# Optimization experiments

Measured on AMD Instinct MI355X. Metric: run time of the kernel, lower is better.

## Reference

```python
import jax, jax.numpy as jnp
import numpy as np

C, H, W = 32, 128, 128

def grid_sample_plane(plane, gx, gy):
    """PyTorch F.grid_sample(mode='bilinear', align_corners=True, padding_mode='zeros').
    plane: (C,H,W); gx,gy: (B,N) in [-1,1] (x indexes W, y indexes H).
    Returns (B,C,N)."""
    x = (gx + 1.0) * 0.5 * (W - 1)
    y = (gy + 1.0) * 0.5 * (H - 1)
    x0 = jnp.floor(x); y0 = jnp.floor(y)
    wx = x - x0; wy = y - y0
    x0i = x0.astype(jnp.int32); y0i = y0.astype(jnp.int32)
    def corner(xi, yi, w):
        valid = (xi >= 0) & (xi < W) & (yi >= 0) & (yi < H)
        xc = jnp.clip(xi, 0, W - 1); yc = jnp.clip(yi, 0, H - 1)
        v = plane[:, yc, xc]            # (C,B,N)
        return v * (w * valid)[None]
    out = (corner(x0i, y0i, (1 - wx) * (1 - wy))
           + corner(x0i + 1, y0i, wx * (1 - wy))
           + corner(x0i, y0i + 1, (1 - wx) * wy)
           + corner(x0i + 1, y0i + 1, wx * wy))   # (C,B,N)
    return jnp.transpose(out, (1, 0, 2))           # (B,C,N)


def setup_inputs() -> dict:
    key = jax.random.key(0)
    ks = jax.random.split(key, 8)
    B, N = 4, 262144
    grid_coords = jax.random.uniform(ks[0], (B, N, 3), jnp.float32, -1.0, 1.0)
    triplanes = jax.random.normal(ks[1], (3 * C, H, W), jnp.float32)
    w0 = jax.random.normal(ks[2], (128, 32), jnp.float32) * (1.0 / np.sqrt(32))
    b0 = jax.random.normal(ks[3], (128,), jnp.float32) * 0.01
    w1 = jax.random.normal(ks[4], (128, 128), jnp.float32) * (1.0 / np.sqrt(128))
    b1 = jax.random.normal(ks[5], (128,), jnp.float32) * 0.01
    w2 = jax.random.normal(ks[6], (4, 128), jnp.float32) * (1.0 / np.sqrt(128))
    b2 = jax.random.normal(ks[7], (4,), jnp.float32) * 0.01
    return {"grid_coords": grid_coords, "triplanes": triplanes,
            "w0": w0, "b0": b0, "w1": w1, "b1": b1, "w2": w2, "b2": b2}


def reference(grid_coords, triplanes, w0, b0, w1, b1, w2, b2):
    B, N, _ = grid_coords.shape
    feat_xy, feat_yz, feat_xz = jnp.split(triplanes, 3, axis=0)
    x = grid_coords[..., 0]; y = grid_coords[..., 1]; z = grid_coords[..., 2]
    # fused tri-plane gather + sum, (B,C,N)
    sampled = (grid_sample_plane(feat_xy, x, y)
               + grid_sample_plane(feat_xz, x, z)
               + grid_sample_plane(feat_yz, y, z))
    # NOTE: the original code does .reshape(batch, -1, channel) on a (B,C,1,N)
    # contiguous tensor (NOT a transpose) -- replicate that exact layout reinterpretation.
    feats = sampled.reshape(B, N, C)
    net = jax.nn.relu(feats @ w0.T + b0)
    net = jax.nn.relu(net @ w1.T + b1)
    net = jax.nn.relu(net @ w2.T + b2)            # (B,N,4)
    # raw = cat(rgb=net[...,1:4], alpha=net[...,0:1]) along channel
    raw = jnp.concatenate([net[..., 1:4], net[..., 0:1]], axis=-1)
    return raw
```

## Files before the change

### kernel.cpp

```cpp
#include <hip/hip_runtime.h>
#include <hip/hip_bf16.h>


#define C_ 32
#define HW_ (128 * 128)
#define HQS 40

typedef short s8v __attribute__((ext_vector_type(8)));
typedef float f4v __attribute__((ext_vector_type(4)));
typedef unsigned int u4v __attribute__((ext_vector_type(4)));
typedef unsigned int u2v __attribute__((ext_vector_type(2)));

__device__ __attribute__((aligned(64))) unsigned short g_planes[3 * HW_ * C_];
__device__ __attribute__((aligned(16))) unsigned short g_w0[128 * 32];
__device__ __attribute__((aligned(16))) unsigned short g_w1[128 * 128];
__device__ __attribute__((aligned(16))) unsigned short g_w2[16 * 128];
__device__ __attribute__((aligned(16))) float g_b0[128];
__device__ __attribute__((aligned(16))) float g_b1[128];
__device__ __attribute__((aligned(16))) float g_b2p[16];

template <typename TO, typename FROM>
static __device__ __forceinline__ TO bitc(FROM f) {
    union { FROM a; TO b; } u; u.a = f; return u.b;
}

template <typename V>
static __device__ __forceinline__ auto mfma_k32(V a, V b, f4v c, int)
    -> decltype(__builtin_amdgcn_mfma_f32_16x16x32_bf16(a, b, c, 0, 0, 0)) {
    return __builtin_amdgcn_mfma_f32_16x16x32_bf16(a, b, c, 0, 0, 0);
}
template <typename V>
static __device__ __forceinline__ f4v mfma_k32(V a, V b, f4v c, long) {
    typedef __bf16 b8v __attribute__((ext_vector_type(8)));
    return __builtin_amdgcn_mfma_f32_16x16x32_bf16(bitc<b8v>(a), bitc<b8v>(b), c, 0, 0, 0);
}
static __device__ __forceinline__ f4v MFMA(s8v a, s8v b, f4v c) {
    return mfma_k32(a, b, c, 0);
}

__device__ __forceinline__ unsigned short f2bf(float f) {
    union { float f; unsigned int i; } v; v.f = f;
    unsigned int r = v.i + 0x7FFFu + ((v.i >> 16) & 1u);
    return (unsigned short)(r >> 16);
}

static __device__ __forceinline__ unsigned int relu_pk(float a, float b) {
    float x = a > 0.0f ? a : 0.0f;
    float y = b > 0.0f ? b : 0.0f;
    unsigned int r;
    asm("v_cvt_pk_bf16_f32 %0, %1, %2" : "=v"(r) : "v"(x), "v"(y));
    return r;
}
static __device__ __forceinline__ unsigned int cvt_pk(float a, float b) {
    unsigned int r;
    asm("v_cvt_pk_bf16_f32 %0, %1, %2" : "=v"(r) : "v"(a), "v"(b));
    return r;
}

__global__ __launch_bounds__(256) void prep_planes_k(const float* __restrict__ tp) {
    __shared__ float buf[32][65];
    const int tid = threadIdx.x;
    const int bid = blockIdx.x;
    const int pl  = bid >> 8;
    const int xy0 = (bid & 255) << 6;
#pragma unroll
    for (int i = 0; i < 8; ++i) {
        int idx = i * 256 + tid;
        int c = idx >> 6, x = idx & 63;
        buf[c][x] = tp[(pl * C_ + c) * HW_ + xy0 + x];
    }
    __syncthreads();
#pragma unroll
    for (int i = 0; i < 8; ++i) {
        int idx = i * 256 + tid;
        int x = idx >> 5, c = idx & 31;
        g_planes[(pl * HW_ + xy0 + x) * C_ + c] = f2bf(buf[c][x]);
    }
}

__global__ void prep_weights_k(const float* __restrict__ w0, const float* __restrict__ b0,
                               const float* __restrict__ w1, const float* __restrict__ b1,
                               const float* __restrict__ w2, const float* __restrict__ b2) {
    int i = blockIdx.x * 256 + threadIdx.x;
    if (i < 128 * 32)  g_w0[i] = f2bf(w0[i]);
    if (i < 128 * 128) g_w1[i] = f2bf(w1[i]);
    if (i < 16 * 128) {
        int n = i >> 7, k = i & 127;
        g_w2[i] = f2bf(n < 4 ? w2[((n + 1) & 3) * 128 + k] : 0.0f);
    }
    if (i < 128) { g_b0[i] = b0[i]; g_b1[i] = b1[i]; }
    if (i < 16)  g_b2p[i] = (i < 4) ? b2[(i + 1) & 3] : 0.0f;
}

static __device__ __forceinline__ void corner8(const unsigned short* __restrict__ rp,
                                               float w, float* facc) {
    const u4v dw = *(const u4v*)rp;
#pragma unroll
    for (int jj = 0; jj < 4; ++jj) {
        facc[2 * jj]     += w * __uint_as_float(dw[jj] << 16);
        facc[2 * jj + 1] += w * __uint_as_float(dw[jj] & 0xFFFF0000u);
    }
}
static __device__ __forceinline__ void plane8(const unsigned short* __restrict__ pb,
                                              int ia, int ib, float wa, float wb,
                                              float* facc) {
    const unsigned short* r0 = pb + (ib * 128 + ia) * C_;
    const unsigned short* r1 = r0 + 128 * C_;
    const float wa0 = 1.0f - wa, wb0 = 1.0f - wb;
    corner8(r0,      wa0 * wb0, facc);
    corner8(r0 + C_, wa  * wb0, facc);
    corner8(r1,      wa0 * wb,  facc);
    corner8(r1 + C_, wa  * wb,  facc);
}

__global__ __launch_bounds__(256) void fused_k(const float* __restrict__ coords,
                                               float* __restrict__ out) {
    __shared__ __attribute__((aligned(16))) unsigned short smem[16384 + 4 * 16 * HQS];
    __shared__ __attribute__((aligned(16))) float lds_bias[256];
    const int tid  = threadIdx.x;
    const int wave = tid >> 6;
    const int lane = tid & 63;
    const int l15  = lane & 15;
    const int quad = lane >> 4;
    const int ch8  = quad * 8;

    const int wg = blockIdx.x;
    const int b  = wg >> 9;
    const int nb = wg & 511;
    const int n0 = nb << 9;

    if (tid < 128) { lds_bias[tid] = g_b0[tid]; lds_bias[128 + tid] = g_b1[tid]; }

    {
        const int qa  = lane & 3;
        const int p15 = lane >> 2;
        const unsigned short* pb0 = g_planes + 0 * (HW_ * C_) + qa * 8;
        const unsigned short* pb1 = g_planes + 1 * (HW_ * C_) + qa * 8;
        const unsigned short* pb2 = g_planes + 2 * (HW_ * C_) + qa * 8;
#pragma unroll 1
        for (int s = 0; s < 8; ++s) {
            const int nl = s * 64 + wave * 16 + p15;
            const float* cp = coords + (size_t)(b * 262144 + n0 + nl) * 3;
            const float gx = cp[0], gy = cp[1], gz = cp[2];

            float fx = (gx + 1.0f) * 63.5f;
            float fy = (gy + 1.0f) * 63.5f;
            float fz = (gz + 1.0f) * 63.5f;
            float xf = fminf(floorf(fx), 126.0f);
            float yf = fminf(floorf(fy), 126.0f);
            float zf = fminf(floorf(fz), 126.0f);
            const float wx = fx - xf, wy = fy - yf, wz = fz - zf;
            const int xi = (int)xf, yi = (int)yf, zi = (int)zf;

            float facc[8];
#pragma unroll
            for (int j = 0; j < 8; ++j) facc[j] = 0.0f;
            plane8(pb0, xi, yi, wx, wy, facc);
            plane8(pb2, xi, zi, wx, wz, facc);
            plane8(pb1, yi, zi, wy, wz, facc);

            const int nlx = nl ^ (qa << 4);
#pragma unroll
            for (int j = 0; j < 4; ++j) {
                const unsigned int p = cvt_pk(facc[2 * j], facc[2 * j + 1]);
                smem[(qa * 8 + 2 * j) * 512 + nlx]     = (unsigned short)p;
                smem[(qa * 8 + 2 * j + 1) * 512 + nlx] = (unsigned short)(p >> 16);
            }
        }
    }
    __syncthreads();

    s8v w0f[8], w1f[4][8], w2f[4];
#pragma unroll
    for (int nt = 0; nt < 8; ++nt)
        w0f[nt] = *(const s8v*)(g_w0 + (nt * 16 + l15) * 32 + ch8);
#pragma unroll
    for (int kc = 0; kc < 4; ++kc)
#pragma unroll
        for (int nt = 0; nt < 8; ++nt)
            w1f[kc][nt] = *(const s8v*)(g_w1 + (nt * 16 + l15) * 128 + kc * 32 + ch8);
#pragma unroll
    for (int kc = 0; kc < 4; ++kc)
        w2f[kc] = *(const s8v*)(g_w2 + l15 * 128 + kc * 32 + ch8);
    const f4v b2v = *(const f4v*)(g_b2p + quad * 4);

    unsigned short* hbq = smem + 16384 + wave * (16 * HQS);
    const int xw = wave << 4;

#pragma unroll 1
    for (int i = 0; i < 8; ++i) {
        const int ci = wave * 8 + i;
        int bo = 0;
        asm volatile("" : "+v"(bo));
        const float* bp = lds_bias + bo;

        const s8v a = *(const s8v*)(smem + ci * 512 + ((l15 * 32 + ch8) ^ xw));

        f4v d[8];
#pragma unroll
        for (int j = 0; j < 8; ++j)
            d[j] = *(const f4v*)(bp + 128 + j * 16 + quad * 4);

#pragma unroll
        for (int kc = 0; kc < 4; ++kc) {
#pragma unroll
            for (int s = 0; s < 2; ++s) {
                const int nt = 2 * kc + s;
                const f4v bi = *(const f4v*)(bp + nt * 16 + quad * 4);
                f4v c1 = MFMA(w0f[nt], a, bi);
                u2v pk;
                pk[0] = relu_pk(c1[0], c1[1]);
                pk[1] = relu_pk(c1[2], c1[3]);
                *(u2v*)(hbq + l15 * HQS + s * 16 + quad * 4) = pk;
            }
            const s8v a2 = *(const s8v*)(hbq + l15 * HQS + ch8);
#pragma unroll
            for (int j = 0; j < 8; ++j)
                d[j] = MFMA(w1f[kc][j], a2, d[j]);
        }

        f4v o = b2v;
#pragma unroll
        for (int kc = 0; kc < 4; ++kc) {
#pragma unroll
            for (int s = 0; s < 2; ++s) {
                const int j = 2 * kc + s;
                u2v pk;
                pk[0] = relu_pk(d[j][0], d[j][1]);
                pk[1] = relu_pk(d[j][2], d[j][3]);
                *(u2v*)(hbq + l15 * HQS + s * 16 + quad * 4) = pk;
            }
            const s8v a3 = *(const s8v*)(hbq + l15 * HQS + ch8);
            o = MFMA(w2f[kc], a3, o);
        }

        if (quad == 0) {
            f4v r;
#pragma unroll
            for (int j = 0; j < 4; ++j) r[j] = o[j] > 0.0f ? o[j] : 0.0f;
            const int t = b * 16384 + ci * 512 + nb;
            *(f4v*)(out + (size_t)(t * 16 + l15) * 4) = r;
        }
    }
}

extern "C" void kernel_launch(void* const* d_in, const int* in_sizes, int n_in,
                              void* d_out, int out_size, void* d_ws, size_t ws_size,
                              hipStream_t stream) {
    const float* coords = (const float*)d_in[0];
    const float* tp = (const float*)d_in[1];
    const float* w0 = (const float*)d_in[2];
    const float* b0 = (const float*)d_in[3];
    const float* w1 = (const float*)d_in[4];
    const float* b1 = (const float*)d_in[5];
    const float* w2 = (const float*)d_in[6];
    const float* b2 = (const float*)d_in[7];
    float* out = (float*)d_out;

    prep_planes_k<<<768, 256, 0, stream>>>(tp);
    prep_weights_k<<<64, 256, 0, stream>>>(w0, b0, w1, b1, w2, b2);
    fused_k<<<2048, 256, 0, stream>>>(coords, out);
}
```

Before: 202.4 us.

## Merge prep kernels, swizzle hidden-activation LDS staging, raise MLP wave priority

Folds the plane-transpose and weight-conversion prep kernels into one launch, with block index selecting the role, to save a kernel launch. Replaces the per-wave hidden-activation staging addresses with an XOR swizzle on both the write and the read side, aimed at reducing LDS bank conflicts. Wraps the MFMA MLP section in s_setprio(1)/s_setprio(0) so waves doing matrix work are scheduled ahead of waves doing gathers. The swizzle must keep write and read mappings consistent, or the hidden activations get mixed up.

```diff
diff --git a/kernel.cpp b/kernel.cpp
--- a/kernel.cpp
+++ b/kernel.cpp
@@ -57,39 +57,43 @@
     return r;
 }
 
-__global__ __launch_bounds__(256) void prep_planes_k(const float* __restrict__ tp) {
+__global__ __launch_bounds__(256) void prep_all_k(const float* __restrict__ tp,
+                                                  const float* __restrict__ w0,
+                                                  const float* __restrict__ b0,
+                                                  const float* __restrict__ w1,
+                                                  const float* __restrict__ b1,
+                                                  const float* __restrict__ w2,
+                                                  const float* __restrict__ b2) {
     __shared__ float buf[32][65];
     const int tid = threadIdx.x;
     const int bid = blockIdx.x;
-    const int pl  = bid >> 8;
-    const int xy0 = (bid & 255) << 6;
-#pragma unroll
-    for (int i = 0; i < 8; ++i) {
-        int idx = i * 256 + tid;
-        int c = idx >> 6, x = idx & 63;
-        buf[c][x] = tp[(pl * C_ + c) * HW_ + xy0 + x];
-    }
-    __syncthreads();
-#pragma unroll
-    for (int i = 0; i < 8; ++i) {
-        int idx = i * 256 + tid;
-        int x = idx >> 5, c = idx & 31;
-        g_planes[(pl * HW_ + xy0 + x) * C_ + c] = f2bf(buf[c][x]);
-    }
-}
-
-__global__ void prep_weights_k(const float* __restrict__ w0, const float* __restrict__ b0,
-                               const float* __restrict__ w1, const float* __restrict__ b1,
-                               const float* __restrict__ w2, const float* __restrict__ b2) {
-    int i = blockIdx.x * 256 + threadIdx.x;
-    if (i < 128 * 32)  g_w0[i] = f2bf(w0[i]);
-    if (i < 128 * 128) g_w1[i] = f2bf(w1[i]);
-    if (i < 16 * 128) {
-        int n = i >> 7, k = i & 127;
-        g_w2[i] = f2bf(n < 4 ? w2[((n + 1) & 3) * 128 + k] : 0.0f);
-    }
-    if (i < 128) { g_b0[i] = b0[i]; g_b1[i] = b1[i]; }
-    if (i < 16)  g_b2p[i] = (i < 4) ? b2[(i + 1) & 3] : 0.0f;
+    if (bid < 768) {
+        const int pl  = bid >> 8;
+        const int xy0 = (bid & 255) << 6;
+#pragma unroll
+        for (int i = 0; i < 8; ++i) {
+            int idx = i * 256 + tid;
+            int c = idx >> 6, x = idx & 63;
+            buf[c][x] = tp[(pl * C_ + c) * HW_ + xy0 + x];
+        }
+        __syncthreads();
+#pragma unroll
+        for (int i = 0; i < 8; ++i) {
+            int idx = i * 256 + tid;
+            int x = idx >> 5, c = idx & 31;
+            g_planes[(pl * HW_ + xy0 + x) * C_ + c] = f2bf(buf[c][x]);
+        }
+    } else {
+        int i = (bid - 768) * 256 + tid;
+        if (i < 128 * 32)  g_w0[i] = f2bf(w0[i]);
+        if (i < 128 * 128) g_w1[i] = f2bf(w1[i]);
+        if (i < 16 * 128) {
+            int n = i >> 7, k = i & 127;
+            g_w2[i] = f2bf(n < 4 ? w2[((n + 1) & 3) * 128 + k] : 0.0f);
+        }
+        if (i < 128) { g_b0[i] = b0[i]; g_b1[i] = b1[i]; }
+        if (i < 16)  g_b2p[i] = (i < 4) ? b2[(i + 1) & 3] : 0.0f;
+    }
 }
 
 static __device__ __forceinline__ void corner8(const unsigned short* __restrict__ rp,
@@ -187,6 +191,11 @@
     unsigned short* hbq = smem + 16384 + wave * (16 * HQS);
     const int xw = wave << 4;
 
+    const int sx  = (l15 >> 1) & 1;
+    const int q2  = quad ^ ((l15 & 1) << 1);
+    const int wof = l15 * HQS + (q2 << 2);
+    const int rof = l15 * HQS + ((quad ^ (l15 & 3)) << 3);
+
 #pragma unroll 1
     for (int i = 0; i < 8; ++i) {
         const int ci = wave * 8 + i;
@@ -195,6 +204,8 @@
         const float* bp = lds_bias + bo;
 
         const s8v a = *(const s8v*)(smem + ci * 512 + ((l15 * 32 + ch8) ^ xw));
+
+        __builtin_amdgcn_s_setprio(1);
 
         f4v d[8];
 #pragma unroll
@@ -211,9 +222,9 @@
                 u2v pk;
                 pk[0] = relu_pk(c1[0], c1[1]);
                 pk[1] = relu_pk(c1[2], c1[3]);
-                *(u2v*)(hbq + l15 * HQS + s * 16 + quad * 4) = pk;
+                *(u2v*)(hbq + wof + ((s ^ sx) << 4)) = pk;
             }
-            const s8v a2 = *(const s8v*)(hbq + l15 * HQS + ch8);
+            const s8v a2 = *(const s8v*)(hbq + rof);
 #pragma unroll
             for (int j = 0; j < 8; ++j)
                 d[j] = MFMA(w1f[kc][j], a2, d[j]);
@@ -228,11 +239,13 @@
                 u2v pk;
                 pk[0] = relu_pk(d[j][0], d[j][1]);
                 pk[1] = relu_pk(d[j][2], d[j][3]);
-                *(u2v*)(hbq + l15 * HQS + s * 16 + quad * 4) = pk;
+                *(u2v*)(hbq + wof + ((s ^ sx) << 4)) = pk;
             }
-            const s8v a3 = *(const s8v*)(hbq + l15 * HQS + ch8);
+            const s8v a3 = *(const s8v*)(hbq + rof);
             o = MFMA(w2f[kc], a3, o);
         }
+
+        __builtin_amdgcn_s_setprio(0);
 
         if (quad == 0) {
             f4v r;
@@ -257,7 +270,6 @@
     const float* b2 = (const float*)d_in[7];
     float* out = (float*)d_out;
 
-    prep_planes_k<<<768, 256, 0, stream>>>(tp);
-    prep_weights_k<<<64, 256, 0, stream>>>(w0, b0, w1, b1, w2, b2);
+    prep_all_k<<<832, 256, 0, stream>>>(tp, w0, b0, w1, b1, w2, b2);
     fused_k<<<2048, 256, 0, stream>>>(coords, out);
 }
```

After: 207.1 us. 1.02x slower.
